# Kernel tuning notes

Measured on AMD Instinct MI355X. Metric: run time of the kernel, lower is better.

Reference implementation:

```python
import jax, jax.numpy as jnp
import numpy as np

EMBED = 1024
HEADS = 16
HDIM = 64
FF = 4 * EMBED
EPS = 1e-5


def layer_norm(x, g, b):
    mu = jnp.mean(x, axis=-1, keepdims=True)
    var = jnp.var(x, axis=-1, keepdims=True)
    return (x - mu) * jax.lax.rsqrt(var + EPS) * g + b


def setup_inputs() -> dict:
    key = jax.random.key(0)
    ks = jax.random.split(key, 12)
    s = lambda fan_in: 1.0 / np.sqrt(fan_in)
    return {
        "x": jax.random.normal(ks[0], (2, 2048, EMBED), jnp.float32),
        "w_qkv": jax.random.uniform(ks[1], (EMBED, 3 * HEADS * HDIM), jnp.float32, -s(EMBED), s(EMBED)),
        "w_proj": jax.random.uniform(ks[2], (HEADS * HDIM, EMBED), jnp.float32, -s(HEADS * HDIM), s(HEADS * HDIM)),
        "b_proj": jax.random.uniform(ks[3], (EMBED,), jnp.float32, -s(HEADS * HDIM), s(HEADS * HDIM)),
        "w1": jax.random.uniform(ks[4], (EMBED, FF), jnp.float32, -s(EMBED), s(EMBED)),
        "b1": jax.random.uniform(ks[5], (FF,), jnp.float32, -s(EMBED), s(EMBED)),
        "w2": jax.random.uniform(ks[6], (FF, EMBED), jnp.float32, -s(FF), s(FF)),
        "b2": jax.random.uniform(ks[7], (EMBED,), jnp.float32, -s(FF), s(FF)),
        "g1": jnp.ones((EMBED,), jnp.float32),
        "be1": jnp.zeros((EMBED,), jnp.float32),
        "g2": jnp.ones((EMBED,), jnp.float32),
        "be2": jnp.zeros((EMBED,), jnp.float32),
    }


def reference(x, w_qkv, w_proj, b_proj, w1, b1, w2, b2, g1, be1, g2, be2):
    bs, seq, _ = x.shape
    # --- MHA on pre-norm ---
    h = layer_norm(x, g1, be1)
    qkv = h @ w_qkv  # [b, s, 3*H*D]
    qkv = qkv.reshape(bs, seq, HEADS, 3, HDIM)
    q = qkv[:, :, :, 0, :]  # [b, s, h, d]
    k = qkv[:, :, :, 1, :]
    v = qkv[:, :, :, 2, :]
    attn = jnp.einsum("bqhd,bkhd->bhqk", q, k) / np.sqrt(HDIM)
    causal = jnp.tril(jnp.ones((seq, seq), bool))
    attn = jnp.where(causal, attn, -jnp.inf)
    attn = jax.nn.softmax(attn, axis=-1)
    out = jnp.einsum("bhqk,bkhd->bhqd", attn, v)
    # Faithful to original bug: .view without transposing heads back.
    out = out.reshape(bs, seq, HEADS * HDIM)
    out = out @ w_proj + b_proj
    x = x + out
    # --- FFN on pre-norm ---
    h2 = layer_norm(x, g2, be2)
    ff = jax.nn.relu(h2 @ w1 + b1) @ w2 + b2
    return x + ff
```

## Files before the change

kernel.cpp:

```cpp
#include <hip/hip_runtime.h>
#include <cstdint>

#define EMBED 1024
#define HEADS 16
#define HDIM  64
#define SEQ   2048
#define BATCH 2
#define ROWS  (BATCH*SEQ)

typedef __bf16 bf16x8 __attribute__((ext_vector_type(8)));
typedef float  f32x4  __attribute__((ext_vector_type(4)));
typedef float  f32x16 __attribute__((ext_vector_type(16)));
typedef unsigned int uint32x2 __attribute__((ext_vector_type(2)));

__device__ __forceinline__ unsigned short f2bf(float f) {
    union { float f; uint32_t u; } v; v.f = f;
    uint32_t r = v.u + 0x7fffu + ((v.u >> 16) & 1u);
    return (unsigned short)(r >> 16);
}

__device__ __forceinline__ uint32_t cvtpk_bf16(float lo, float hi) {
    uint32_t r;
    asm("v_cvt_pk_bf16_f32 %0, %1, %2" : "=v"(r) : "v"(lo), "v"(hi));
    return r;
}

__device__ __forceinline__ float fexp2(float x) {
    float r;
    asm("v_exp_f32 %0, %1" : "=v"(r) : "v"(x));
    return r;
}

#define GLDS(src, dst) __builtin_amdgcn_global_load_lds( \
    (const __attribute__((address_space(1))) uint32_t*)(src), \
    (__attribute__((address_space(3))) uint32_t*)(dst), 16, 0, 0)

__global__ __launch_bounds__(256) void k_transpose_bf16(
    const float* __restrict__ in, unsigned short* __restrict__ out, int K, int N)
{
    __shared__ float tile[32][33];
    const int tx = threadIdx.x & 31, ty = threadIdx.x >> 5;
    const int n0 = blockIdx.x * 32, k0 = blockIdx.y * 32;
#pragma unroll
    for (int r = 0; r < 4; ++r)
        tile[ty + 8*r][tx] = in[(size_t)(k0 + ty + 8*r) * N + n0 + tx];
    __syncthreads();
#pragma unroll
    for (int r = 0; r < 4; ++r)
        out[(size_t)(n0 + ty + 8*r) * K + k0 + tx] = f2bf(tile[tx][ty + 8*r]);
}

__global__ __launch_bounds__(256) void k_layernorm(
    const float* __restrict__ x, const float* __restrict__ g, const float* __restrict__ b,
    unsigned short* __restrict__ h)
{
    const int row = blockIdx.x, t = threadIdx.x;
    float4 v = ((const float4*)(x + (size_t)row * EMBED))[t];
    float s = v.x + v.y + v.z + v.w;
    float q = v.x*v.x + v.y*v.y + v.z*v.z + v.w*v.w;
#pragma unroll
    for (int off = 32; off >= 1; off >>= 1) {
        s += __shfl_xor(s, off, 64);
        q += __shfl_xor(q, off, 64);
    }
    __shared__ float ss[4], sq[4];
    if ((t & 63) == 0) { ss[t >> 6] = s; sq[t >> 6] = q; }
    __syncthreads();
    s = ss[0] + ss[1] + ss[2] + ss[3];
    q = sq[0] + sq[1] + sq[2] + sq[3];
    const float mu  = s * (1.0f / EMBED);
    const float var = q * (1.0f / EMBED) - mu * mu;
    const float rs  = rsqrtf(var + 1e-5f);
    float4 gv = ((const float4*)g)[t];
    float4 bv = ((const float4*)b)[t];
    ushort4 o;
    o.x = f2bf((v.x - mu) * rs * gv.x + bv.x);
    o.y = f2bf((v.y - mu) * rs * gv.y + bv.y);
    o.z = f2bf((v.z - mu) * rs * gv.z + bv.z);
    o.w = f2bf((v.w - mu) * rs * gv.w + bv.w);
    ((ushort4*)(h + (size_t)row * EMBED))[t] = o;
}

template<int FLAGS, typename OutT>
__global__ __launch_bounds__(512) void k_gemm_bt(
    const unsigned short* __restrict__ A,
    const unsigned short* __restrict__ BT,
    const float* __restrict__ bias,
    const float* __restrict__ resid,
    OutT* __restrict__ C,
    int M, int N, int K)
{
    __shared__ uint4 ldsv[4096];
    char* aL = (char*)ldsv;
    char* bL = aL + 16384;
    const int t = threadIdx.x, l = t & 63, w = t >> 6;
    const int wr = w >> 1, wc = w & 1;
    const int g = l >> 4, c = l & 15;

    const int gx = gridDim.x;
    const int lin = blockIdx.y * gx + blockIdx.x;
    const int cpx = (gx * gridDim.y) >> 3;
    const int swz = (lin & 7) * cpx + (lin >> 3);
    const int row0 = (swz / gx) * 128, col0 = (swz % gx) * 128;

    const int swc = (((l & 7) ^ (l >> 3)) * 8);
    const int rA0 = w*16 + (l >> 3), rA1 = rA0 + 8;
    const unsigned short* aS0 = A  + (size_t)(row0 + rA0) * K + swc;
    const unsigned short* aS1 = A  + (size_t)(row0 + rA1) * K + swc;
    const unsigned short* bS0 = BT + (size_t)(col0 + rA0) * K + swc;
    const unsigned short* bS1 = BT + (size_t)(col0 + rA1) * K + swc;
    const int dst0 = w * 2048, dst1 = w * 2048 + 1024;

    f32x4 acc[2][4];
#pragma unroll
    for (int m = 0; m < 2; ++m)
#pragma unroll
        for (int n = 0; n < 4; ++n) acc[m][n] = f32x4{0.f, 0.f, 0.f, 0.f};

    auto stage = [&](int kt, int bo) {
        const size_t ko = (size_t)kt * 64;
        GLDS(aS0 + ko, aL + bo + dst0);
        GLDS(aS1 + ko, aL + bo + dst1);
        GLDS(bS0 + ko, bL + bo + dst0);
        GLDS(bS1 + ko, bL + bo + dst1);
    };
    auto compute = [&](int bo) {
#pragma unroll
        for (int ks = 0; ks < 2; ++ks) {
            const int chb = ((ks*4 + g) ^ (c & 7)) * 16;
            bf16x8 af[2], bfr[4];
#pragma unroll
            for (int m = 0; m < 2; ++m)
                af[m] = *(const bf16x8*)(aL + bo + (wr*32 + m*16 + c) * 128 + chb);
#pragma unroll
            for (int n = 0; n < 4; ++n)
                bfr[n] = *(const bf16x8*)(bL + bo + (wc*64 + n*16 + c) * 128 + chb);
            __builtin_amdgcn_s_setprio(1);
#pragma unroll
            for (int m = 0; m < 2; ++m)
#pragma unroll
                for (int n = 0; n < 4; ++n)
                    acc[m][n] = __builtin_amdgcn_mfma_f32_16x16x32_bf16(af[m], bfr[n], acc[m][n], 0, 0, 0);
            __builtin_amdgcn_s_setprio(0);
        }
    };

    const int nkt = K >> 6;
    stage(0, 0);
    int bufo = 0;
    for (int kt = 0; kt < nkt - 1; ++kt) {
        stage(kt + 1, bufo ^ 32768);
        asm volatile("s_waitcnt vmcnt(4)" ::: "memory");
        __builtin_amdgcn_s_barrier();
        compute(bufo);
        asm volatile("s_waitcnt lgkmcnt(0)" ::: "memory");
        __builtin_amdgcn_s_barrier();
        bufo ^= 32768;
    }
    asm volatile("s_waitcnt vmcnt(0)" ::: "memory");
    __builtin_amdgcn_s_barrier();
    compute(bufo);

#pragma unroll
    for (int m = 0; m < 2; ++m) {
        const int rb = row0 + wr*32 + m*16 + g*4;
#pragma unroll
        for (int n = 0; n < 4; ++n) {
            const int col = col0 + wc*64 + n*16 + c;
            float bv = 0.f;
            if constexpr ((FLAGS & 1) != 0) bv = bias[col];
#pragma unroll
            for (int j = 0; j < 4; ++j) {
                float v = acc[m][n][j] + bv;
                if constexpr ((FLAGS & 2) != 0) v = fmaxf(v, 0.f);
                if constexpr ((FLAGS & 4) != 0) v += resid[(size_t)(rb + j) * N + col];
                if constexpr (sizeof(OutT) == 2) C[(size_t)(rb + j) * N + col] = (OutT)f2bf(v);
                else                             C[(size_t)(rb + j) * N + col] = v;
            }
        }
    }
}

template<int FLAGS, typename OutT>
__global__ __launch_bounds__(512) __attribute__((amdgpu_waves_per_eu(2, 2)))
void k_gemm256(
    const unsigned short* __restrict__ A,
    const unsigned short* __restrict__ BT,
    const float* __restrict__ bias,
    OutT* __restrict__ C,
    unsigned short* __restrict__ Qo,
    unsigned short* __restrict__ Ko,
    unsigned short* __restrict__ Vo,
    int M, int N, int K)
{
    __shared__ uint4 ldsv[8192];
    char* base = (char*)ldsv;
    const int t = threadIdx.x, l = t & 63, w = t >> 6;
    const int wr = w >> 2, wc = w & 3;
    const int g = l >> 4, c = l & 15;

    const int gx = gridDim.x;
    const int lin = blockIdx.y * gx + blockIdx.x;
    const int cpx = (gx * gridDim.y) >> 3;
    const int swz = (lin & 7) * cpx + (lin >> 3);
    const int row0 = (swz / gx) * 256, col0 = (swz % gx) * 256;

    const int sr = l >> 3, sc = l & 7;
    const int swk = (sc ^ sr) * 8;
    const unsigned short* aSr = A  + (size_t)(row0 + w*32 + sr) * K + swk;
    const unsigned short* bSr = BT + (size_t)(col0 + w*32 + sr) * K + swk;

    f32x4 acc[8][4];
#pragma unroll
    for (int m = 0; m < 8; ++m)
#pragma unroll
        for (int n = 0; n < 4; ++n) acc[m][n] = f32x4{0.f, 0.f, 0.f, 0.f};

    auto stage = [&](int kt, int bo) {
        const size_t ko = (size_t)kt * 64;
#pragma unroll
        for (int i = 0; i < 4; ++i) {
            GLDS(aSr + ko + (size_t)(i*8) * K, base + bo + (w*4 + i)*1024);
            GLDS(bSr + ko + (size_t)(i*8) * K, base + bo + 32768 + (w*4 + i)*1024);
        }
    };

    const int nkt = K >> 6;
    stage(0, 0);
    asm volatile("s_waitcnt vmcnt(0)" ::: "memory");
    __builtin_amdgcn_s_barrier();
    int bufo = 0;
    for (int kt = 0; kt < nkt; ++kt) {
        if (kt + 1 < nkt) stage(kt + 1, bufo ^ 65536);
        bf16x8 bfr[4][2];
#pragma unroll
        for (int n = 0; n < 4; ++n)
#pragma unroll
            for (int ks = 0; ks < 2; ++ks) {
                const int r = wc*64 + n*16 + c;
                bfr[n][ks] = *(const bf16x8*)(base + bufo + 32768 + r*128
                                              + (((ks*4 + g) ^ (c & 7)) * 16));
            }
#pragma unroll
        for (int p = 0; p < 4; ++p) {
            bf16x8 af[2][2];
#pragma unroll
            for (int mi = 0; mi < 2; ++mi)
#pragma unroll
                for (int ks = 0; ks < 2; ++ks) {
                    const int r = wr*128 + (p*2 + mi)*16 + c;
                    af[mi][ks] = *(const bf16x8*)(base + bufo + r*128
                                                  + (((ks*4 + g) ^ (c & 7)) * 16));
                }
            __builtin_amdgcn_s_setprio(1);
#pragma unroll
            for (int ks = 0; ks < 2; ++ks)
#pragma unroll
                for (int mi = 0; mi < 2; ++mi)
#pragma unroll
                    for (int n = 0; n < 4; ++n)
                        acc[p*2 + mi][n] = __builtin_amdgcn_mfma_f32_16x16x32_bf16(
                            af[mi][ks], bfr[n][ks], acc[p*2 + mi][n], 0, 0, 0);
            __builtin_amdgcn_s_setprio(0);
        }
        if (kt + 1 < nkt) {
            asm volatile("s_waitcnt vmcnt(0)" ::: "memory");
            __builtin_amdgcn_s_barrier();
            bufo ^= 65536;
        }
    }

    if constexpr ((FLAGS & 8) != 0) {
#pragma unroll
        for (int m = 0; m < 8; ++m) {
            const int rb = row0 + wr*128 + m*16 + g*4;
            const int b  = rb >> 11;
            const int q0 = rb & 2047;
#pragma unroll
            for (int n = 0; n < 4; ++n) {
                const int col = col0 + wc*64 + n*16 + c;
                const int hh  = col / 192;
                const int rem = col - hh * 192;
                const int tt  = rem >> 6;
                const int d   = rem & 63;
                const int bhh = b * HEADS + hh;
                if (tt == 2) {
                    const int st_e = q0 >> 6, kk = q0 & 63;
                    const int f_e  = (d >> 5) * 4 + (kk >> 4);
                    const int ln_e = ((kk >> 3) & 1) * 32 + (d & 31);
                    const int e0   = kk & 7;
                    ushort4 o;
                    o.x = f2bf(acc[m][n][0]); o.y = f2bf(acc[m][n][1]);
                    o.z = f2bf(acc[m][n][2]); o.w = f2bf(acc[m][n][3]);
                    *(ushort4*)(Vo + (size_t)bhh * (SEQ*HDIM) + st_e*4096 + f_e*512 + ln_e*8 + e0) = o;
                } else if (tt == 1) {
                    const int st_e = q0 >> 6;
                    const int f_e  = ((q0 >> 5) & 1) * 4 + (d >> 4);
                    const int lq_e = q0 & 31;
                    const int ln_b = ((d >> 3) & 1) * 32;
                    const int e_e  = d & 7;
                    unsigned short* dst = Ko + (size_t)bhh * (SEQ*HDIM) + st_e*4096 + f_e*512
                                             + (ln_b + lq_e)*8 + e_e;
#pragma unroll
                    for (int j = 0; j < 4; ++j)
                        dst[j*8] = f2bf(acc[m][n][j]);
                } else {
                    unsigned short* dst = Qo + ((size_t)bhh * SEQ + q0) * HDIM + d;
#pragma unroll
                    for (int j = 0; j < 4; ++j)
                        dst[(size_t)j * HDIM] = f2bf(acc[m][n][j]);
                }
            }
        }
    } else {
#pragma unroll
        for (int m = 0; m < 8; ++m) {
            const int rb = row0 + wr*128 + m*16 + g*4;
#pragma unroll
            for (int n = 0; n < 4; ++n) {
                const int col = col0 + wc*64 + n*16 + c;
                float bv = 0.f;
                if constexpr ((FLAGS & 1) != 0) bv = bias[col];
#pragma unroll
                for (int j = 0; j < 4; ++j) {
                    float v = acc[m][n][j] + bv;
                    if constexpr ((FLAGS & 2) != 0) v = fmaxf(v, 0.f);
                    if constexpr (sizeof(OutT) == 2) C[(size_t)(rb + j) * N + col] = (OutT)f2bf(v);
                    else                             C[(size_t)(rb + j) * N + col] = v;
                }
            }
        }
    }
}

__global__ __launch_bounds__(512) __attribute__((amdgpu_waves_per_eu(2, 2)))
void k_attention(
    const unsigned short* __restrict__ Qb,
    const unsigned short* __restrict__ Kf,
    const unsigned short* __restrict__ Vf,
    unsigned short* __restrict__ out)
{
    const int t = threadIdx.x, l = t & 63, w = t >> 6;
    const int lq = l & 31, hi = l >> 5;
    const int bid = blockIdx.x;
    const int sbid = (bid & 7) * 32 + (bid >> 3);
    const int bh = sbid >> 3, j = sbid & 7;
    const int qb = (w < 4) ? (4*j + w) : (63 - 4*j - (w - 4));
    const int q  = qb * 32 + lq;

    const unsigned short* Qh  = Qb + (size_t)bh * SEQ * HDIM;
    const unsigned short* Kfh = Kf + (size_t)bh * SEQ * HDIM + l*8;
    const unsigned short* Vfh = Vf + (size_t)bh * SEQ * HDIM + l*8;

    const bf16x8 qf0 = *(const bf16x8*)(Qh + (size_t)q * HDIM      + hi*8);
    const bf16x8 qf1 = *(const bf16x8*)(Qh + (size_t)q * HDIM + 16 + hi*8);
    const bf16x8 qf2 = *(const bf16x8*)(Qh + (size_t)q * HDIM + 32 + hi*8);
    const bf16x8 qf3 = *(const bf16x8*)(Qh + (size_t)q * HDIM + 48 + hi*8);

    f32x16 oT0, oT1;
#pragma unroll
    for (int i = 0; i < 16; ++i) { oT0[i] = 0.f; oT1[i] = 0.f; }
    float lacc0 = 0.f, lacc1 = 0.f, lacc2 = 0.f, lacc3 = 0.f;
    const float kSc = 0.18033688011112042f;
    const int nst = (qb >> 1) + 1;

    bf16x8 kA0, kA1, kA2, kA3, kA4, kA5, kA6, kA7;
    bf16x8 kB0, kB1, kB2, kB3, kB4, kB5, kB6, kB7;

#define LOADK(stv, KF) do {                                                     \
    const unsigned short* kp_ = Kfh + (size_t)(stv) * 4096;                     \
    KF##0 = *(const bf16x8*)(kp_ +    0); KF##1 = *(const bf16x8*)(kp_ +  512); \
    KF##2 = *(const bf16x8*)(kp_ + 1024); KF##3 = *(const bf16x8*)(kp_ + 1536); \
    KF##4 = *(const bf16x8*)(kp_ + 2048); KF##5 = *(const bf16x8*)(kp_ + 2560); \
    KF##6 = *(const bf16x8*)(kp_ + 3072); KF##7 = *(const bf16x8*)(kp_ + 3584); \
} while (0)

#define STEP(stv, KF) do {                                                      \
    const int kv0_ = (stv) * 64;                                                \
    const unsigned short* vp_ = Vfh + (size_t)(stv) * 4096;                     \
    bf16x8 vf0_ = *(const bf16x8*)(vp_ +    0), vf1_ = *(const bf16x8*)(vp_ +  512); \
    bf16x8 vf2_ = *(const bf16x8*)(vp_ + 1024), vf3_ = *(const bf16x8*)(vp_ + 1536); \
    bf16x8 vf4_ = *(const bf16x8*)(vp_ + 2048), vf5_ = *(const bf16x8*)(vp_ + 2560); \
    bf16x8 vf6_ = *(const bf16x8*)(vp_ + 3072), vf7_ = *(const bf16x8*)(vp_ + 3584); \
    f32x16 sA_, sB_;                                                            \
    _Pragma("unroll")                                                           \
    for (int i = 0; i < 16; ++i) { sA_[i] = 0.f; sB_[i] = 0.f; }               \
    __builtin_amdgcn_s_setprio(1);                                              \
    sA_ = __builtin_amdgcn_mfma_f32_32x32x16_bf16(KF##0, qf0, sA_, 0, 0, 0);    \
    sA_ = __builtin_amdgcn_mfma_f32_32x32x16_bf16(KF##1, qf1, sA_, 0, 0, 0);    \
    sA_ = __builtin_amdgcn_mfma_f32_32x32x16_bf16(KF##2, qf2, sA_, 0, 0, 0);    \
    sA_ = __builtin_amdgcn_mfma_f32_32x32x16_bf16(KF##3, qf3, sA_, 0, 0, 0);    \
    sB_ = __builtin_amdgcn_mfma_f32_32x32x16_bf16(KF##4, qf0, sB_, 0, 0, 0);    \
    sB_ = __builtin_amdgcn_mfma_f32_32x32x16_bf16(KF##5, qf1, sB_, 0, 0, 0);    \
    sB_ = __builtin_amdgcn_mfma_f32_32x32x16_bf16(KF##6, qf2, sB_, 0, 0, 0);    \
    sB_ = __builtin_amdgcn_mfma_f32_32x32x16_bf16(KF##7, qf3, sB_, 0, 0, 0);    \
    __builtin_amdgcn_s_setprio(0);                                              \
    float p_[32];                                                               \
    if ((stv) == nst - 1) {                                                     \
        _Pragma("unroll")                                                       \
        for (int r = 0; r < 16; ++r) {                                          \
            const int key_ = kv0_ + (r & 3) + 8*(r >> 2) + 4*hi;                \
            p_[r]      = (key_      <= q) ? fexp2(sA_[r] * kSc) : 0.f;          \
            p_[16 + r] = (key_ + 32 <= q) ? fexp2(sB_[r] * kSc) : 0.f;          \
        }                                                                       \
    } else {                                                                    \
        _Pragma("unroll")                                                       \
        for (int r = 0; r < 16; ++r) {                                          \
            p_[r]      = fexp2(sA_[r] * kSc);                                   \
            p_[16 + r] = fexp2(sB_[r] * kSc);                                   \
        }                                                                       \
    }                                                                           \
    _Pragma("unroll")                                                           \
    for (int i = 0; i < 32; i += 4) {                                           \
        lacc0 += p_[i]; lacc1 += p_[i+1]; lacc2 += p_[i+2]; lacc3 += p_[i+3];   \
    }                                                                           \
    bf16x8 pa_[4];                                                              \
    _Pragma("unroll")                                                           \
    for (int ks = 0; ks < 4; ++ks) {                                            \
        const int b8_ = ks * 8;                                                 \
        uint32x2 rA_ = __builtin_amdgcn_permlane32_swap(                        \
            cvtpk_bf16(p_[b8_+0], p_[b8_+1]), cvtpk_bf16(p_[b8_+4], p_[b8_+5]), false, false); \
        uint32x2 rB_ = __builtin_amdgcn_permlane32_swap(                        \
            cvtpk_bf16(p_[b8_+2], p_[b8_+3]), cvtpk_bf16(p_[b8_+6], p_[b8_+7]), false, false); \
        union { uint32_t u[4]; bf16x8 v; } pk_;                                 \
        pk_.u[0] = rA_[0]; pk_.u[1] = rB_[0]; pk_.u[2] = rA_[1]; pk_.u[3] = rB_[1]; \
        pa_[ks] = pk_.v;                                                        \
    }                                                                           \
    __builtin_amdgcn_s_setprio(1);                                              \
    oT0 = __builtin_amdgcn_mfma_f32_32x32x16_bf16(vf0_, pa_[0], oT0, 0, 0, 0);  \
    oT0 = __builtin_amdgcn_mfma_f32_32x32x16_bf16(vf1_, pa_[1], oT0, 0, 0, 0);  \
    oT0 = __builtin_amdgcn_mfma_f32_32x32x16_bf16(vf2_, pa_[2], oT0, 0, 0, 0);  \
    oT0 = __builtin_amdgcn_mfma_f32_32x32x16_bf16(vf3_, pa_[3], oT0, 0, 0, 0);  \
    oT1 = __builtin_amdgcn_mfma_f32_32x32x16_bf16(vf4_, pa_[0], oT1, 0, 0, 0);  \
    oT1 = __builtin_amdgcn_mfma_f32_32x32x16_bf16(vf5_, pa_[1], oT1, 0, 0, 0);  \
    oT1 = __builtin_amdgcn_mfma_f32_32x32x16_bf16(vf6_, pa_[2], oT1, 0, 0, 0);  \
    oT1 = __builtin_amdgcn_mfma_f32_32x32x16_bf16(vf7_, pa_[3], oT1, 0, 0, 0);  \
    __builtin_amdgcn_s_setprio(0);                                              \
} while (0)

    LOADK(0, kA);
    int st = 0;
    for (;;) {
        if (st + 1 < nst) LOADK(st + 1, kB);
        STEP(st, kA);
        if (++st >= nst) break;
        if (st + 1 < nst) LOADK(st + 1, kA);
        STEP(st, kB);
        if (++st >= nst) break;
    }
#undef LOADK
#undef STEP

    float lsum = (lacc0 + lacc1) + (lacc2 + lacc3);
    lsum += __shfl_xor(lsum, 32, 64);
    const float inv = 1.f / lsum;
    unsigned short* ob = out + ((size_t)bh * SEQ + q) * HDIM;
#pragma unroll
    for (int m2 = 0; m2 < 4; ++m2) {
        ushort4 o0, o1;
        o0.x = f2bf(oT0[m2*4+0] * inv); o0.y = f2bf(oT0[m2*4+1] * inv);
        o0.z = f2bf(oT0[m2*4+2] * inv); o0.w = f2bf(oT0[m2*4+3] * inv);
        o1.x = f2bf(oT1[m2*4+0] * inv); o1.y = f2bf(oT1[m2*4+1] * inv);
        o1.z = f2bf(oT1[m2*4+2] * inv); o1.w = f2bf(oT1[m2*4+3] * inv);
        *(ushort4*)(ob +      m2*8 + hi*4) = o0;
        *(ushort4*)(ob + 32 + m2*8 + hi*4) = o1;
    }
}

extern "C" void kernel_launch(void* const* d_in, const int* in_sizes, int n_in,
                              void* d_out, int out_size, void* d_ws, size_t ws_size,
                              hipStream_t stream)
{
    (void)in_sizes; (void)n_in; (void)out_size; (void)ws_size;
    const float* x      = (const float*)d_in[0];
    const float* w_qkv  = (const float*)d_in[1];
    const float* w_proj = (const float*)d_in[2];
    const float* b_proj = (const float*)d_in[3];
    const float* w1     = (const float*)d_in[4];
    const float* b1     = (const float*)d_in[5];
    const float* w2     = (const float*)d_in[6];
    const float* b2     = (const float*)d_in[7];
    const float* g1     = (const float*)d_in[8];
    const float* be1    = (const float*)d_in[9];
    const float* g2     = (const float*)d_in[10];
    const float* be2    = (const float*)d_in[11];

    char* ws = (char*)d_ws;
    size_t o = 0;
    auto take = [&](size_t bytes) -> char* {
        char* p = ws + o;
        o += (bytes + 255) & ~(size_t)255;
        return p;
    };
    unsigned short* wqkvT  = (unsigned short*)take(3072ull * 1024 * 2);
    unsigned short* wprojT = (unsigned short*)take(1024ull * 1024 * 2);
    unsigned short* w1T    = (unsigned short*)take(4096ull * 1024 * 2);
    unsigned short* w2T    = (unsigned short*)take(1024ull * 4096 * 2);
    unsigned short* h      = (unsigned short*)take(4096ull * 1024 * 2);
    unsigned short* Qb     = (unsigned short*)take(4096ull * 1024 * 2);
    unsigned short* Kfb    = (unsigned short*)take(4096ull * 1024 * 2);
    unsigned short* Vfb    = (unsigned short*)take(4096ull * 1024 * 2);
    unsigned short* attno  = (unsigned short*)take(4096ull * 1024 * 2);
    float*          x2     = (float*)take(4096ull * 1024 * 4);
    unsigned short* f1     = Qb;

    k_transpose_bf16<<<dim3(96, 32),  256, 0, stream>>>(w_qkv,  wqkvT,  1024, 3072);
    k_transpose_bf16<<<dim3(32, 32),  256, 0, stream>>>(w_proj, wprojT, 1024, 1024);
    k_transpose_bf16<<<dim3(128, 32), 256, 0, stream>>>(w1,     w1T,    1024, 4096);
    k_transpose_bf16<<<dim3(32, 128), 256, 0, stream>>>(w2,     w2T,    4096, 1024);

    k_layernorm<<<4096, 256, 0, stream>>>(x, g1, be1, h);
    k_gemm256<8, unsigned short><<<dim3(12, 16), 512, 0, stream>>>(
        h, wqkvT, nullptr, (unsigned short*)nullptr, Qb, Kfb, Vfb, ROWS, 3072, 1024);
    k_attention<<<256, 512, 0, stream>>>(Qb, Kfb, Vfb, attno);
    k_gemm_bt<5, float><<<dim3(8, 32), 512, 0, stream>>>(
        attno, wprojT, b_proj, x, x2, ROWS, 1024, 1024);
    k_layernorm<<<4096, 256, 0, stream>>>(x2, g2, be2, h);
    k_gemm256<3, unsigned short><<<dim3(16, 16), 512, 0, stream>>>(
        h, w1T, b1, f1, nullptr, nullptr, nullptr, ROWS, 4096, 1024);
    k_gemm_bt<5, float><<<dim3(8, 32), 512, 0, stream>>>(
        f1, w2T, b2, x2, (float*)d_out, ROWS, 1024, 4096);
}
```

Measured before the change: 188.5 us.

## Split-K the FFN down-projection GEMM with 256x256 tiles and a reduce pass

Replaces the final FFN down-projection GEMM (K=4096) with a 4-way split-K kernel using 256x256 tiles, so there are 256 blocks of K=1024 each. Split 0 adds the bias and residual and writes to the output, while splits 1 to 3 write fp32 partials. A separate kernel then sums the partials into the output. This trades larger, more reuse-friendly tiles for three extra fp32 partial buffers and an extra reduction launch. The first partial buffer reuses workspace left over from the already-consumed transposed weights.

Result: slower. 226.9 us (+20.3%).

```diff
diff --git a/kernel.cpp b/kernel.cpp
--- a/kernel.cpp
+++ b/kernel.cpp
@@ -330,6 +330,130 @@
                 }
             }
         }
+    }
+}
+
+__global__ __launch_bounds__(512) __attribute__((amdgpu_waves_per_eu(2, 2)))
+void k_gemm256sk(
+    const unsigned short* __restrict__ A,
+    const unsigned short* __restrict__ BT,
+    const float* __restrict__ bias,
+    const float* __restrict__ resid,
+    float* __restrict__ C0,
+    float* __restrict__ P1, float* __restrict__ P2, float* __restrict__ P3,
+    int M, int N, int K, int lda)
+{
+    __shared__ uint4 ldsv[8192];
+    char* base = (char*)ldsv;
+    const int t = threadIdx.x, l = t & 63, w = t >> 6;
+    const int wr = w >> 2, wc = w & 3;
+    const int g = l >> 4, c = l & 15;
+    const int kz = blockIdx.z;
+
+    const int gx = gridDim.x;
+    const int lin = blockIdx.y * gx + blockIdx.x;
+    const int cpx = (gx * gridDim.y) >> 3;
+    const int swz = (lin & 7) * cpx + (lin >> 3);
+    const int row0 = (swz / gx) * 256, col0 = (swz % gx) * 256;
+
+    const int sr = l >> 3, sc = l & 7;
+    const int swk = (sc ^ sr) * 8;
+    const unsigned short* aSr = A  + (size_t)(row0 + w*32 + sr) * lda + (size_t)kz * K + swk;
+    const unsigned short* bSr = BT + (size_t)(col0 + w*32 + sr) * lda + (size_t)kz * K + swk;
+
+    f32x4 acc[8][4];
+#pragma unroll
+    for (int m = 0; m < 8; ++m)
+#pragma unroll
+        for (int n = 0; n < 4; ++n) acc[m][n] = f32x4{0.f, 0.f, 0.f, 0.f};
+
+    auto stage = [&](int kt, int bo) {
+        const size_t ko = (size_t)kt * 64;
+#pragma unroll
+        for (int i = 0; i < 4; ++i) {
+            GLDS(aSr + ko + (size_t)(i*8) * lda, base + bo + (w*4 + i)*1024);
+            GLDS(bSr + ko + (size_t)(i*8) * lda, base + bo + 32768 + (w*4 + i)*1024);
+        }
+    };
+
+    const int nkt = K >> 6;
+    stage(0, 0);
+    asm volatile("s_waitcnt vmcnt(0)" ::: "memory");
+    __builtin_amdgcn_s_barrier();
+    int bufo = 0;
+    for (int kt = 0; kt < nkt; ++kt) {
+        if (kt + 1 < nkt) stage(kt + 1, bufo ^ 65536);
+        bf16x8 bfr[4][2];
+#pragma unroll
+        for (int n = 0; n < 4; ++n)
+#pragma unroll
+            for (int ks = 0; ks < 2; ++ks) {
+                const int r = wc*64 + n*16 + c;
+                bfr[n][ks] = *(const bf16x8*)(base + bufo + 32768 + r*128
+                                              + (((ks*4 + g) ^ (c & 7)) * 16));
+            }
+#pragma unroll
+        for (int p = 0; p < 4; ++p) {
+            bf16x8 af[2][2];
+#pragma unroll
+            for (int mi = 0; mi < 2; ++mi)
+#pragma unroll
+                for (int ks = 0; ks < 2; ++ks) {
+                    const int r = wr*128 + (p*2 + mi)*16 + c;
+                    af[mi][ks] = *(const bf16x8*)(base + bufo + r*128
+                                                  + (((ks*4 + g) ^ (c & 7)) * 16));
+                }
+            __builtin_amdgcn_s_setprio(1);
+#pragma unroll
+            for (int ks = 0; ks < 2; ++ks)
+#pragma unroll
+                for (int mi = 0; mi < 2; ++mi)
+#pragma unroll
+                    for (int n = 0; n < 4; ++n)
+                        acc[p*2 + mi][n] = __builtin_amdgcn_mfma_f32_16x16x32_bf16(
+                            af[mi][ks], bfr[n][ks], acc[p*2 + mi][n], 0, 0, 0);
+            __builtin_amdgcn_s_setprio(0);
+        }
+        if (kt + 1 < nkt) {
+            asm volatile("s_waitcnt vmcnt(0)" ::: "memory");
+            __builtin_amdgcn_s_barrier();
+            bufo ^= 65536;
+        }
+    }
+
+    float* Cz = (kz == 0) ? C0 : (kz == 1) ? P1 : (kz == 2) ? P2 : P3;
+#pragma unroll
+    for (int m = 0; m < 8; ++m) {
+        const int rb = row0 + wr*128 + m*16 + g*4;
+#pragma unroll
+        for (int n = 0; n < 4; ++n) {
+            const int col = col0 + wc*64 + n*16 + c;
+            const float bv = (kz == 0) ? bias[col] : 0.f;
+#pragma unroll
+            for (int j = 0; j < 4; ++j) {
+                float v = acc[m][n][j] + bv;
+                if (kz == 0) v += resid[(size_t)(rb + j) * N + col];
+                Cz[(size_t)(rb + j) * N + col] = v;
+            }
+        }
+    }
+}
+
+__global__ __launch_bounds__(256) void k_reduceadd3(
+    float* __restrict__ C, const float* __restrict__ P1,
+    const float* __restrict__ P2, const float* __restrict__ P3, int n4)
+{
+    const int stride = gridDim.x * 256;
+    for (int i = blockIdx.x * 256 + threadIdx.x; i < n4; i += stride) {
+        float4 a = ((const float4*)C)[i];
+        const float4 b = ((const float4*)P1)[i];
+        const float4 c = ((const float4*)P2)[i];
+        const float4 d = ((const float4*)P3)[i];
+        a.x += b.x + c.x + d.x;
+        a.y += b.y + c.y + d.y;
+        a.z += b.z + c.z + d.z;
+        a.w += b.w + c.w + d.w;
+        ((float4*)C)[i] = a;
     }
 }
 
@@ -503,6 +627,9 @@
     unsigned short* attno  = (unsigned short*)take(4096ull * 1024 * 2);
     float*          x2     = (float*)take(4096ull * 1024 * 4);
     unsigned short* f1     = Qb;
+    float*          p1     = (float*)ws;
+    float*          p2     = (float*)take(4096ull * 1024 * 4);
+    float*          p3     = (float*)take(4096ull * 1024 * 4);
 
     k_transpose_bf16<<<dim3(96, 32),  256, 0, stream>>>(w_qkv,  wqkvT,  1024, 3072);
     k_transpose_bf16<<<dim3(32, 32),  256, 0, stream>>>(w_proj, wprojT, 1024, 1024);
@@ -518,6 +645,7 @@
     k_layernorm<<<4096, 256, 0, stream>>>(x2, g2, be2, h);
     k_gemm256<3, unsigned short><<<dim3(16, 16), 512, 0, stream>>>(
         h, w1T, b1, f1, nullptr, nullptr, nullptr, ROWS, 4096, 1024);
-    k_gemm_bt<5, float><<<dim3(8, 32), 512, 0, stream>>>(
-        f1, w2T, b2, x2, (float*)d_out, ROWS, 1024, 4096);
-}
+    k_gemm256sk<<<dim3(4, 16, 4), 512, 0, stream>>>(
+        f1, w2T, b2, x2, (float*)d_out, p1, p2, p3, ROWS, 1024, 1024, 4096);
+    k_reduceadd3<<<2048, 256, 0, stream>>>((float*)d_out, p1, p2, p3, ROWS * 1024 / 4);
+}
```

## Deepen GEMM LDS pipeline from double to quad buffering

Applied to the files above, without the earlier changes.

Raises the GEMM's shared-memory staging from two buffers to four (128 KB LDS), prefetching three K-tiles ahead with matching vmcnt waits. The aim is to hide more global-memory latency behind MFMA compute. The cost is that the larger LDS footprint limits each CU to one 512-thread block, which reduces occupancy and latency hiding across blocks.

After: 190.6 us. No clear change (+1.1%).

```diff
diff --git a/kernel.cpp b/kernel.cpp
--- a/kernel.cpp
+++ b/kernel.cpp
@@ -90,9 +90,8 @@
     OutT* __restrict__ C,
     int M, int N, int K)
 {
-    __shared__ uint4 ldsv[4096];
-    char* aL = (char*)ldsv;
-    char* bL = aL + 16384;
+    __shared__ uint4 ldsv[8192];
+    char* base = (char*)ldsv;
     const int t = threadIdx.x, l = t & 63, w = t >> 6;
     const int wr = w >> 1, wc = w & 1;
     const int g = l >> 4, c = l & 15;
@@ -119,10 +118,10 @@
 
     auto stage = [&](int kt, int bo) {
         const size_t ko = (size_t)kt * 64;
-        GLDS(aS0 + ko, aL + bo + dst0);
-        GLDS(aS1 + ko, aL + bo + dst1);
-        GLDS(bS0 + ko, bL + bo + dst0);
-        GLDS(bS1 + ko, bL + bo + dst1);
+        GLDS(aS0 + ko, base + bo + dst0);
+        GLDS(aS1 + ko, base + bo + dst1);
+        GLDS(bS0 + ko, base + bo + 16384 + dst0);
+        GLDS(bS1 + ko, base + bo + 16384 + dst1);
     };
     auto compute = [&](int bo) {
 #pragma unroll
@@ -131,10 +130,10 @@
             bf16x8 af[2], bfr[4];
 #pragma unroll
             for (int m = 0; m < 2; ++m)
-                af[m] = *(const bf16x8*)(aL + bo + (wr*32 + m*16 + c) * 128 + chb);
+                af[m] = *(const bf16x8*)(base + bo + (wr*32 + m*16 + c) * 128 + chb);
 #pragma unroll
             for (int n = 0; n < 4; ++n)
-                bfr[n] = *(const bf16x8*)(bL + bo + (wc*64 + n*16 + c) * 128 + chb);
+                bfr[n] = *(const bf16x8*)(base + bo + 16384 + (wc*64 + n*16 + c) * 128 + chb);
             __builtin_amdgcn_s_setprio(1);
 #pragma unroll
             for (int m = 0; m < 2; ++m)
@@ -147,19 +146,24 @@
 
     const int nkt = K >> 6;
     stage(0, 0);
-    int bufo = 0;
-    for (int kt = 0; kt < nkt - 1; ++kt) {
-        stage(kt + 1, bufo ^ 32768);
-        asm volatile("s_waitcnt vmcnt(4)" ::: "memory");
+    stage(1, 32768);
+    stage(2, 65536);
+    for (int kt = 0; kt < nkt; ++kt) {
+        const int bo = (kt & 3) * 32768;
+        if (kt + 3 < nkt) {
+            stage(kt + 3, ((kt + 3) & 3) * 32768);
+            asm volatile("s_waitcnt vmcnt(12)" ::: "memory");
+        } else {
+            const int rem = nkt - 1 - kt;
+            if (rem >= 2)      asm volatile("s_waitcnt vmcnt(8)" ::: "memory");
+            else if (rem == 1) asm volatile("s_waitcnt vmcnt(4)" ::: "memory");
+            else               asm volatile("s_waitcnt vmcnt(0)" ::: "memory");
+        }
         __builtin_amdgcn_s_barrier();
-        compute(bufo);
+        compute(bo);
         asm volatile("s_waitcnt lgkmcnt(0)" ::: "memory");
         __builtin_amdgcn_s_barrier();
-        bufo ^= 32768;
-    }
-    asm volatile("s_waitcnt vmcnt(0)" ::: "memory");
-    __builtin_amdgcn_s_barrier();
-    compute(bufo);
+    }
 
 #pragma unroll
     for (int m = 0; m < 2; ++m) {
```

## Split-K the FFN down-projection GEMM with a separate reduction pass

Applied to the files above, without the earlier changes.

The final K=4096 GEMM now splits its K dimension across two grid z-slices. Slice 0 writes the biased, residual-added result and slice 1 writes raw fp32 partials into a scratch buffer at the start of the workspace. A new elementwise kernel then adds the partials into the output. This doubles the block count of a long-K GEMM so more CUs stay busy, at the cost of 16MB of extra fp32 traffic plus one more kernel launch. The scratch buffer reuses weight-transpose space that is dead by that point in the pipeline.

Result: slower. 199.8 us (+6.0%).

```diff
diff --git a/kernel.cpp b/kernel.cpp
--- a/kernel.cpp
+++ b/kernel.cpp
@@ -81,13 +81,14 @@
     ((ushort4*)(h + (size_t)row * EMBED))[t] = o;
 }
 
-template<int FLAGS, typename OutT>
+template<int FLAGS, int KS, typename OutT>
 __global__ __launch_bounds__(512) void k_gemm_bt(
     const unsigned short* __restrict__ A,
     const unsigned short* __restrict__ BT,
     const float* __restrict__ bias,
     const float* __restrict__ resid,
     OutT* __restrict__ C,
+    float* __restrict__ P,
     int M, int N, int K)
 {
     __shared__ uint4 ldsv[4096];
@@ -103,12 +104,16 @@
     const int swz = (lin & 7) * cpx + (lin >> 3);
     const int row0 = (swz / gx) * 128, col0 = (swz % gx) * 128;
 
+    const int Kd = K / KS;
+    const int kz = (KS > 1) ? blockIdx.z : 0;
+    const int kof = kz * Kd;
+
     const int swc = (((l & 7) ^ (l >> 3)) * 8);
     const int rA0 = w*16 + (l >> 3), rA1 = rA0 + 8;
-    const unsigned short* aS0 = A  + (size_t)(row0 + rA0) * K + swc;
-    const unsigned short* aS1 = A  + (size_t)(row0 + rA1) * K + swc;
-    const unsigned short* bS0 = BT + (size_t)(col0 + rA0) * K + swc;
-    const unsigned short* bS1 = BT + (size_t)(col0 + rA1) * K + swc;
+    const unsigned short* aS0 = A  + (size_t)(row0 + rA0) * K + kof + swc;
+    const unsigned short* aS1 = A  + (size_t)(row0 + rA1) * K + kof + swc;
+    const unsigned short* bS0 = BT + (size_t)(col0 + rA0) * K + kof + swc;
+    const unsigned short* bS1 = BT + (size_t)(col0 + rA1) * K + kof + swc;
     const int dst0 = w * 2048, dst1 = w * 2048 + 1024;
 
     f32x4 acc[2][4];
@@ -145,7 +150,7 @@
         }
     };
 
-    const int nkt = K >> 6;
+    const int nkt = Kd >> 6;
     stage(0, 0);
     int bufo = 0;
     for (int kt = 0; kt < nkt - 1; ++kt) {
@@ -161,23 +166,49 @@
     __builtin_amdgcn_s_barrier();
     compute(bufo);
 
-#pragma unroll
-    for (int m = 0; m < 2; ++m) {
-        const int rb = row0 + wr*32 + m*16 + g*4;
-#pragma unroll
-        for (int n = 0; n < 4; ++n) {
-            const int col = col0 + wc*64 + n*16 + c;
-            float bv = 0.f;
-            if constexpr ((FLAGS & 1) != 0) bv = bias[col];
-#pragma unroll
-            for (int j = 0; j < 4; ++j) {
-                float v = acc[m][n][j] + bv;
-                if constexpr ((FLAGS & 2) != 0) v = fmaxf(v, 0.f);
-                if constexpr ((FLAGS & 4) != 0) v += resid[(size_t)(rb + j) * N + col];
-                if constexpr (sizeof(OutT) == 2) C[(size_t)(rb + j) * N + col] = (OutT)f2bf(v);
-                else                             C[(size_t)(rb + j) * N + col] = v;
+    if (KS == 1 || kz == 0) {
+#pragma unroll
+        for (int m = 0; m < 2; ++m) {
+            const int rb = row0 + wr*32 + m*16 + g*4;
+#pragma unroll
+            for (int n = 0; n < 4; ++n) {
+                const int col = col0 + wc*64 + n*16 + c;
+                float bv = 0.f;
+                if constexpr ((FLAGS & 1) != 0) bv = bias[col];
+#pragma unroll
+                for (int j = 0; j < 4; ++j) {
+                    float v = acc[m][n][j] + bv;
+                    if constexpr ((FLAGS & 2) != 0) v = fmaxf(v, 0.f);
+                    if constexpr ((FLAGS & 4) != 0) v += resid[(size_t)(rb + j) * N + col];
+                    if constexpr (sizeof(OutT) == 2) C[(size_t)(rb + j) * N + col] = (OutT)f2bf(v);
+                    else                             C[(size_t)(rb + j) * N + col] = v;
+                }
             }
         }
+    } else {
+#pragma unroll
+        for (int m = 0; m < 2; ++m) {
+            const int rb = row0 + wr*32 + m*16 + g*4;
+#pragma unroll
+            for (int n = 0; n < 4; ++n) {
+                const int col = col0 + wc*64 + n*16 + c;
+#pragma unroll
+                for (int j = 0; j < 4; ++j)
+                    P[(size_t)(rb + j) * N + col] = acc[m][n][j];
+            }
+        }
+    }
+}
+
+__global__ __launch_bounds__(256) void k_reduceadd1(
+    float* __restrict__ C, const float* __restrict__ P1, int n4)
+{
+    const int stride = gridDim.x * 256;
+    for (int i = blockIdx.x * 256 + threadIdx.x; i < n4; i += stride) {
+        float4 a = ((const float4*)C)[i];
+        const float4 b = ((const float4*)P1)[i];
+        a.x += b.x; a.y += b.y; a.z += b.z; a.w += b.w;
+        ((float4*)C)[i] = a;
     }
 }
 
@@ -503,6 +534,7 @@
     unsigned short* attno  = (unsigned short*)take(4096ull * 1024 * 2);
     float*          x2     = (float*)take(4096ull * 1024 * 4);
     unsigned short* f1     = Qb;
+    float*          p1     = (float*)ws;
 
     k_transpose_bf16<<<dim3(96, 32),  256, 0, stream>>>(w_qkv,  wqkvT,  1024, 3072);
     k_transpose_bf16<<<dim3(32, 32),  256, 0, stream>>>(w_proj, wprojT, 1024, 1024);
@@ -513,11 +545,12 @@
     k_gemm256<8, unsigned short><<<dim3(12, 16), 512, 0, stream>>>(
         h, wqkvT, nullptr, (unsigned short*)nullptr, Qb, Kfb, Vfb, ROWS, 3072, 1024);
     k_attention<<<256, 512, 0, stream>>>(Qb, Kfb, Vfb, attno);
-    k_gemm_bt<5, float><<<dim3(8, 32), 512, 0, stream>>>(
-        attno, wprojT, b_proj, x, x2, ROWS, 1024, 1024);
+    k_gemm_bt<5, 1, float><<<dim3(8, 32), 512, 0, stream>>>(
+        attno, wprojT, b_proj, x, x2, nullptr, ROWS, 1024, 1024);
     k_layernorm<<<4096, 256, 0, stream>>>(x2, g2, be2, h);
     k_gemm256<3, unsigned short><<<dim3(16, 16), 512, 0, stream>>>(
         h, w1T, b1, f1, nullptr, nullptr, nullptr, ROWS, 4096, 1024);
-    k_gemm_bt<5, float><<<dim3(8, 32), 512, 0, stream>>>(
-        f1, w2T, b2, x2, (float*)d_out, ROWS, 1024, 4096);
-}
+    k_gemm_bt<5, 2, float><<<dim3(8, 32, 2), 512, 0, stream>>>(
+        f1, w2T, b2, x2, (float*)d_out, p1, ROWS, 1024, 4096);
+    k_reduceadd1<<<2048, 256, 0, stream>>>((float*)d_out, p1, ROWS * 1024 / 4);
+}
```
